# Kernel optimization log

Hardware: AMD Instinct MI355X
Metric: run time of the kernel (lower is better)

## Reference

```python
import jax, jax.numpy as jnp
import numpy as np

N, E, F, H, G, C = 50000, 600000, 128, 128, 500, 10
BN_EPS = 1e-5

def setup_inputs() -> dict:
    key = jax.random.key(0)
    ks = jax.random.split(key, 20)
    def lin(k, fan_in, shape):
        b = 1.0 / np.sqrt(fan_in)
        return jax.random.uniform(k, shape, jnp.float32, -b, b)
    inp = {
        'x': jax.random.normal(ks[0], (N, F), jnp.float32),
        'edge_index': jax.random.randint(ks[1], (2, E), 0, N, jnp.int64),
        'batch': jnp.sort(jax.random.randint(ks[2], (N,), 0, G, jnp.int64)),
        # conv1 MLP: Linear(F,H) -> BN(H) -> ReLU -> Dropout -> Linear(H,H) -> ReLU
        'W1a': lin(ks[3], F, (F, H)), 'b1a': lin(ks[4], F, (H,)),
        'g1': jnp.ones((H,), jnp.float32), 'be1': jnp.zeros((H,), jnp.float32),
        'm1': jnp.zeros((H,), jnp.float32), 'v1': jnp.ones((H,), jnp.float32),
        'W1b': lin(ks[5], H, (H, H)), 'b1b': lin(ks[6], H, (H,)),
        # conv2 MLP: Linear(H,H) -> ReLU -> BN(H) -> Dropout -> Linear(H,H) -> ReLU
        'W2a': lin(ks[7], H, (H, H)), 'b2a': lin(ks[8], H, (H,)),
        'g2': jnp.ones((H,), jnp.float32), 'be2': jnp.zeros((H,), jnp.float32),
        'm2': jnp.zeros((H,), jnp.float32), 'v2': jnp.ones((H,), jnp.float32),
        'W2b': lin(ks[9], H, (H, H)), 'b2b': lin(ks[10], H, (H,)),
        # heads
        'Wl1': lin(ks[11], 2 * H, (2 * H, H // 2)), 'bl1': lin(ks[12], 2 * H, (H // 2,)),
        'Wl2': lin(ks[13], H // 2, (H // 2, C)), 'bl2': lin(ks[14], H // 2, (C,)),
    }
    return inp

def _bn(h, g, b, m, v):
    return (h - m) * (g / jnp.sqrt(v + BN_EPS)) + b

def _gin_aggregate(x, src, dst):
    # out[i] = x[i] + sum_{j->i} x[j]  (GINConv with eps=0)
    return x + jax.ops.segment_sum(x[src], dst, num_segments=N)

def reference(x, edge_index, batch,
              W1a, b1a, g1, be1, m1, v1, W1b, b1b,
              W2a, b2a, g2, be2, m2, v2, W2b, b2b,
              Wl1, bl1, Wl2, bl2):
    src, dst = edge_index[0], edge_index[1]
    # conv1
    a1 = _gin_aggregate(x, src, dst)                       # [N, F]
    h1 = _bn(a1 @ W1a + b1a, g1, be1, m1, v1)
    h1 = jax.nn.relu(h1)                                   # dropout = identity (eval)
    h1 = jax.nn.relu(h1 @ W1b + b1b)                       # [N, H]
    # conv2
    a2 = _gin_aggregate(h1, src, dst)                      # [N, H]
    h2 = jax.nn.relu(a2 @ W2a + b2a)
    h2 = _bn(h2, g2, be2, m2, v2)
    h2 = jax.nn.relu(h2 @ W2b + b2b)                       # [N, H]
    # global add pool per graph
    p1 = jax.ops.segment_sum(h1, batch, num_segments=G)    # [G, H]
    p2 = jax.ops.segment_sum(h2, batch, num_segments=G)    # [G, H]
    z = jnp.concatenate((p1, p2), axis=1)                  # [G, 2H]
    z = jax.nn.relu(z @ Wl1 + bl1)
    return z @ Wl2 + bl2                                   # [G, C]
```

## Files before the change

kernel.cpp:

```cpp
#include <hip/hip_runtime.h>

#define N_NODES 50000
#define N_EDGES 600000
#define HDIM 128
#define NGRAPH 500
#define NCLASS 10
#define BN_EPS 1e-5f
#define KSLOT 64
#define KSTRIDE 72

typedef short short8 __attribute__((ext_vector_type(8)));
typedef unsigned short ushort8v __attribute__((ext_vector_type(8)));
typedef float floatx4 __attribute__((ext_vector_type(4)));

__device__ __forceinline__ float bf2f(unsigned short u) {
    unsigned int v = ((unsigned int)u) << 16;
    return __uint_as_float(v);
}
__device__ __forceinline__ unsigned short f2bf(float f) {
    unsigned int u = __float_as_uint(f);
    unsigned int r = (u + 0x7fffu + ((u >> 16) & 1u)) >> 16;
    return (unsigned short)r;
}

__global__ void k_zero(int* __restrict__ cnt) {
    int i = blockIdx.x * blockDim.x + threadIdx.x;
    if (i < N_NODES) cnt[i] = 0;
}

#define ILV 13
#define NB_SCAT 586
#define NB_CAST 6250
#define NB_PREPW 256
#define NB_POOLZ 500
#define NB_SETUP (NB_SCAT * ILV)

__global__ void k_setup(const float* __restrict__ x, unsigned short* __restrict__ xb,
                        const int* __restrict__ src, const int* __restrict__ dst,
                        int* __restrict__ cnt, unsigned short* __restrict__ adj,
                        float* __restrict__ pool,
                        const float* __restrict__ W1a, const float* __restrict__ W1b,
                        const float* __restrict__ W2a, const float* __restrict__ W2b,
                        unsigned short* __restrict__ wpack,
                        const float* __restrict__ b1a, const float* __restrict__ g1,
                        const float* __restrict__ be1, const float* __restrict__ m1,
                        const float* __restrict__ v1, const float* __restrict__ b1b,
                        const float* __restrict__ b2a, const float* __restrict__ g2,
                        const float* __restrict__ be2, const float* __restrict__ m2,
                        const float* __restrict__ v2, const float* __restrict__ b2b,
                        float* __restrict__ ep) {
    int b = blockIdx.x;
    int t = threadIdx.x;
    if (b % ILV == 0) {
        int i4 = (b / ILV) * 256 + t;
        if (i4 < N_EDGES / 4) {
            int4 s4 = ((const int4*)src)[i4];
            int4 d4 = ((const int4*)dst)[i4];
            int p;
            p = atomicAdd(&cnt[d4.x], 1); if (p < KSLOT) adj[d4.x * KSTRIDE + p] = (unsigned short)s4.x;
            p = atomicAdd(&cnt[d4.y], 1); if (p < KSLOT) adj[d4.y * KSTRIDE + p] = (unsigned short)s4.y;
            p = atomicAdd(&cnt[d4.z], 1); if (p < KSLOT) adj[d4.z * KSTRIDE + p] = (unsigned short)s4.z;
            p = atomicAdd(&cnt[d4.w], 1); if (p < KSLOT) adj[d4.w * KSTRIDE + p] = (unsigned short)s4.w;
        }
        return;
    }
    b = b - b / ILV - 1;
    if (b < NB_CAST) {
        int i = b * 256 + t;
        float4 v = ((const float4*)x)[i];
        ushort4 o;
        o.x = f2bf(v.x); o.y = f2bf(v.y); o.z = f2bf(v.z); o.w = f2bf(v.w);
        ((ushort4*)xb)[i] = o;
        return;
    }
    b -= NB_CAST;
    if (b < NB_PREPW) {
        int e = b * 256 + t;
        int w = e >> 14;
        int s_ = e & 16383;
        int j = s_ & 7;
        int m = (s_ >> 3) & 15;
        int q = (s_ >> 7) & 3;
        int ks = (s_ >> 9) & 3;
        int ct = (s_ >> 11) & 7;
        int n = ct * 16 + m;
        int k;
        float scale = 1.f;
        if (w == 0 || w == 2) {
            k = ks * 32 + q * 8 + j;
        } else {
            k = (ks * 2 + (j >> 2)) * 16 + q * 4 + (j & 3);
            if (w == 3) scale = g2[k] * rsqrtf(v2[k] + BN_EPS);
        }
        const float* W = (w == 0) ? W1a : (w == 1) ? W1b : (w == 2) ? W2a : W2b;
        wpack[e] = f2bf(W[k * 128 + n] * scale);
        return;
    }
    b -= NB_PREPW;
    if (b < NB_POOLZ) {
        int i = b * 256 + t;
        pool[i] = 0.f;
        return;
    }
    b -= NB_POOLZ;
    if (b != 0) return;
    if (t < 128) {
        int j = t;
        float s1 = g1[j] * rsqrtf(v1[j] + BN_EPS);
        ep[0 * 256 + 0 + j]   = s1;
        ep[0 * 256 + 128 + j] = (b1a[j] - m1[j]) * s1 + be1[j];
        ep[1 * 256 + 0 + j]   = 1.f;
        ep[1 * 256 + 128 + j] = b2a[j];
        ep[512 + j] = b1b[j];
        float acc = b2b[j];
        for (int k = 0; k < 128; k++) {
            float s2k = g2[k] * rsqrtf(v2[k] + BN_EPS);
            acc += (be2[k] - m2[k] * s2k) * W2b[k * 128 + j];
        }
        ep[512 + 128 + j] = acc;
    }
}

__global__ __launch_bounds__(256) void k_agg(const unsigned short* __restrict__ x,
                                             const int* __restrict__ cnt,
                                             const unsigned short* __restrict__ adj,
                                             unsigned short* __restrict__ out) {
    int g = blockIdx.x * 256 + threadIdx.x;
    int node = g >> 4;
    int m = g & 15;
    if (node >= N_NODES) return;

    int len = cnt[node];
    if (len > KSLOT) len = KSLOT;
    const unsigned short* ad = adj + node * KSTRIDE;

    ushort8v ra = *(const ushort8v*)(ad);

    float self[8];
    {
        short8 sv = *(const short8*)(x + (size_t)node * 128 + m * 8);
        #pragma unroll
        for (int j = 0; j < 8; j++) self[j] = bf2f((unsigned short)sv[j]);
    }
    float acc[8];
    #pragma unroll
    for (int j = 0; j < 8; j++) acc[j] = self[j];

    int nb = (len + 7) >> 3;
    for (int b = 0; b < nb; b++) {
        int i = b * 8;
        ushort8v na = *(const ushort8v*)(ad + i + 8);
        int u0 = (i + 0 < len) ? (int)ra[0] : node;
        int u1 = (i + 1 < len) ? (int)ra[1] : node;
        int u2 = (i + 2 < len) ? (int)ra[2] : node;
        int u3 = (i + 3 < len) ? (int)ra[3] : node;
        int u4 = (i + 4 < len) ? (int)ra[4] : node;
        int u5 = (i + 5 < len) ? (int)ra[5] : node;
        int u6 = (i + 6 < len) ? (int)ra[6] : node;
        int u7 = (i + 7 < len) ? (int)ra[7] : node;
        short8 f0 = *(const short8*)(x + (size_t)u0 * 128 + m * 8);
        short8 f1 = *(const short8*)(x + (size_t)u1 * 128 + m * 8);
        short8 f2 = *(const short8*)(x + (size_t)u2 * 128 + m * 8);
        short8 f3 = *(const short8*)(x + (size_t)u3 * 128 + m * 8);
        short8 f4 = *(const short8*)(x + (size_t)u4 * 128 + m * 8);
        short8 f5 = *(const short8*)(x + (size_t)u5 * 128 + m * 8);
        short8 f6 = *(const short8*)(x + (size_t)u6 * 128 + m * 8);
        short8 f7 = *(const short8*)(x + (size_t)u7 * 128 + m * 8);
        #pragma unroll
        for (int j = 0; j < 8; j++) {
            float a = bf2f((unsigned short)f0[j]) + bf2f((unsigned short)f1[j]) +
                      bf2f((unsigned short)f2[j]) + bf2f((unsigned short)f3[j]);
            float c = bf2f((unsigned short)f4[j]) + bf2f((unsigned short)f5[j]) +
                      bf2f((unsigned short)f6[j]) + bf2f((unsigned short)f7[j]);
            acc[j] += a + c;
        }
        ra = na;
    }
    float extra = (float)(nb * 8 - len);
    #pragma unroll
    for (int j = 0; j < 8; j++) acc[j] -= extra * self[j];

    short8 r;
    #pragma unroll
    for (int j = 0; j < 8; j++) r[j] = (short)f2bf(acc[j]);
    *(short8*)(out + (size_t)node * 128 + m * 8) = r;
}

__global__ __launch_bounds__(256, 2) void k_mlp(const unsigned short* __restrict__ A,
                                                const unsigned short* __restrict__ WaP,
                                                const unsigned short* __restrict__ WbP,
                                                const float* __restrict__ epi,
                                                const float* __restrict__ epf,
                                                const int* __restrict__ batch,
                                                float* __restrict__ poolc,
                                                unsigned short* __restrict__ Out, int n) {
    __shared__ unsigned short Wl[2][16384];
    __shared__ float ps[16][132];
    int t = threadIdx.x;
    int lane = t & 63;
    int w = t >> 6;
    int q = lane >> 4;
    int m = lane & 15;

    int rowbase0 = blockIdx.x * 64;
    int base = rowbase0 + w * 16;
    int node = base + m;
    if (node >= n) node = n - 1;

    short8 a1[4];
    #pragma unroll
    for (int s = 0; s < 4; s++)
        a1[s] = *(const short8*)(A + (size_t)node * 128 + s * 32 + q * 8);

    #pragma unroll
    for (int i = 0; i < 8; i++) {
        int c = t + 256 * i;
        *(short8*)(&Wl[0][c * 8]) = *(const short8*)(WaP + c * 8);
        *(short8*)(&Wl[1][c * 8]) = *(const short8*)(WbP + c * 8);
    }
    __syncthreads();

    int lbase = lane * 8;

    floatx4 acc1[8];
    #pragma unroll
    for (int c = 0; c < 8; c++) acc1[c] = (floatx4)0.f;
    #pragma unroll
    for (int s = 0; s < 4; s++) {
        #pragma unroll
        for (int ct = 0; ct < 8; ct++) {
            short8 wf = *(const short8*)(&Wl[0][(ct * 4 + s) * 512 + lbase]);
            acc1[ct] = __builtin_amdgcn_mfma_f32_16x16x32_bf16(wf, a1[s], acc1[ct], 0, 0, 0);
        }
    }

    short8 a2[4];
    #pragma unroll
    for (int s = 0; s < 4; s++) {
        #pragma unroll
        for (int j = 0; j < 8; j++) {
            int ct = s * 2 + (j >> 2);
            int r = j & 3;
            int col = ct * 16 + q * 4 + r;
            float P = epi[col], Q = epi[128 + col];
            float v = fmaxf(fmaf(acc1[ct][r], P, Q), 0.f);
            a2[s][j] = (short)f2bf(v);
        }
    }

    floatx4 acc2[8];
    #pragma unroll
    for (int c = 0; c < 8; c++) acc2[c] = (floatx4)0.f;
    #pragma unroll
    for (int s = 0; s < 4; s++) {
        #pragma unroll
        for (int ct = 0; ct < 8; ct++) {
            short8 wf = *(const short8*)(&Wl[1][(ct * 4 + s) * 512 + lbase]);
            acc2[ct] = __builtin_amdgcn_mfma_f32_16x16x32_bf16(a2[s], wf, acc2[ct], 0, 0, 0);
        }
    }

    #pragma unroll
    for (int ct = 0; ct < 8; ct++) {
        float Qf = epf[ct * 16 + m];
        #pragma unroll
        for (int r = 0; r < 4; r++) acc2[ct][r] = fmaxf(acc2[ct][r] + Qf, 0.f);
    }

    if (Out) {
        #pragma unroll
        for (int ct = 0; ct < 8; ct++) {
            int col = ct * 16 + m;
            #pragma unroll
            for (int r = 0; r < 4; r++) {
                int gr = base + q * 4 + r;
                if (gr < n)
                    Out[(size_t)gr * 128 + col] = f2bf(acc2[ct][r]);
            }
        }
    }

    int mygid[4];
    #pragma unroll
    for (int r = 0; r < 4; r++) {
        int gr = base + q * 4 + r;
        mygid[r] = (gr < n) ? batch[gr] : -1;
    }
    int lastrow = rowbase0 + 63;
    if (lastrow > n - 1) lastrow = n - 1;
    int g0 = batch[rowbase0];
    int g1 = batch[lastrow];
    for (int g = g0; g <= g1; g++) {
        float pv[8];
        #pragma unroll
        for (int ct = 0; ct < 8; ct++) pv[ct] = 0.f;
        #pragma unroll
        for (int r = 0; r < 4; r++) {
            if (mygid[r] == g) {
                #pragma unroll
                for (int ct = 0; ct < 8; ct++) pv[ct] += acc2[ct][r];
            }
        }
        #pragma unroll
        for (int ct = 0; ct < 8; ct++) ps[w * 4 + q][ct * 16 + m] = pv[ct];
        __syncthreads();
        if (t < 128) {
            float s = 0.f;
            #pragma unroll
            for (int k = 0; k < 16; k++) s += ps[k][t];
            atomicAdd(&poolc[g * 256 + t], s);
        }
        __syncthreads();
    }
}

__global__ void k_head(const float* __restrict__ pool, const float* __restrict__ Wl1,
                       const float* __restrict__ bl1, const float* __restrict__ Wl2,
                       const float* __restrict__ bl2, float* __restrict__ out) {
    int g = blockIdx.x;
    int t = threadIdx.x;
    __shared__ float zmid[64];
    const float* z = pool + g * 256;
    float acc = bl1[t];
    #pragma unroll 8
    for (int k = 0; k < 256; k++) acc = fmaf(z[k], Wl1[k * 64 + t], acc);
    zmid[t] = fmaxf(acc, 0.f);
    __syncthreads();
    if (t < NCLASS) {
        float a = bl2[t];
        #pragma unroll
        for (int j = 0; j < 64; j++) a = fmaf(zmid[j], Wl2[j * 10 + t], a);
        out[g * NCLASS + t] = a;
    }
}


extern "C" void kernel_launch(void* const* d_in, const int* in_sizes, int n_in,
                              void* d_out, int out_size, void* d_ws, size_t ws_size,
                              hipStream_t stream) {
    const float* x   = (const float*)d_in[0];
    const int* eidx  = (const int*)d_in[1];
    const int* batch = (const int*)d_in[2];
    const float* W1a = (const float*)d_in[3];
    const float* b1a = (const float*)d_in[4];
    const float* g1  = (const float*)d_in[5];
    const float* be1 = (const float*)d_in[6];
    const float* m1  = (const float*)d_in[7];
    const float* v1  = (const float*)d_in[8];
    const float* W1b = (const float*)d_in[9];
    const float* b1b = (const float*)d_in[10];
    const float* W2a = (const float*)d_in[11];
    const float* b2a = (const float*)d_in[12];
    const float* g2  = (const float*)d_in[13];
    const float* be2 = (const float*)d_in[14];
    const float* m2  = (const float*)d_in[15];
    const float* v2  = (const float*)d_in[16];
    const float* W2b = (const float*)d_in[17];
    const float* b2b = (const float*)d_in[18];
    const float* Wl1 = (const float*)d_in[19];
    const float* bl1 = (const float*)d_in[20];
    const float* Wl2 = (const float*)d_in[21];
    const float* bl2 = (const float*)d_in[22];
    const int* srcv = eidx;
    const int* dstv = eidx + N_EDGES;

    char* ws = (char*)d_ws;
    size_t off = 0;
    auto alloc = [&](size_t bytes) -> void* {
        void* p = ws + off;
        off = (off + bytes + 255) & ~(size_t)255;
        return p;
    };
    int* cnt      = (int*)alloc(sizeof(int) * N_NODES);
    unsigned short* adj = (unsigned short*)alloc(sizeof(unsigned short) * (size_t)N_NODES * KSTRIDE);
    float* ep     = (float*)alloc(sizeof(float) * 768);
    float* pool   = (float*)alloc(sizeof(float) * NGRAPH * 256);
    unsigned short* wpack = (unsigned short*)alloc(sizeof(unsigned short) * 4 * 16384);
    unsigned short* xb    = (unsigned short*)alloc(sizeof(unsigned short) * (size_t)N_NODES * HDIM);
    unsigned short* bufA  = (unsigned short*)alloc(sizeof(unsigned short) * (size_t)N_NODES * HDIM);
    unsigned short* bufC  = (unsigned short*)alloc(sizeof(unsigned short) * (size_t)N_NODES * HDIM);
    (void)ws_size; (void)in_sizes; (void)n_in; (void)out_size;

    float* outp = (float*)d_out;

    k_zero<<<dim3((N_NODES + 255) / 256), dim3(256), 0, stream>>>(cnt);
    k_setup<<<dim3(NB_SETUP), dim3(256), 0, stream>>>(
        x, xb, srcv, dstv, cnt, adj, pool, W1a, W1b, W2a, W2b, wpack,
        b1a, g1, be1, m1, v1, b1b, b2a, g2, be2, m2, v2, b2b, ep);

    dim3 agrid((N_NODES * 16 + 255) / 256), ablk(256);
    dim3 mgrid((N_NODES + 63) / 64), mblk(256);

    k_agg<<<agrid, ablk, 0, stream>>>(xb, cnt, adj, bufA);
    k_mlp<<<mgrid, mblk, 0, stream>>>(bufA, wpack + 0 * 16384, wpack + 1 * 16384,
                                      ep + 0, ep + 512, batch, pool + 0, bufC, N_NODES);
    k_agg<<<agrid, ablk, 0, stream>>>(bufC, cnt, adj, bufA);
    k_mlp<<<mgrid, mblk, 0, stream>>>(bufA, wpack + 2 * 16384, wpack + 3 * 16384,
                                      ep + 256, ep + 640, batch, pool + 128, nullptr, N_NODES);
    k_head<<<dim3(NGRAPH), dim3(64), 0, stream>>>(pool, Wl1, bl1, Wl2, bl2, outp);
}
```

Before: 229.2 us.

## Bucket adjacency lists by source range and batch four nodes per aggregation thread

Adjacency is now split into four buckets per destination, keyed on source node range, each holding at most 28 slots in a 128-entry row. The aggregation kernel runs a fixed grid of 1024 blocks, and each 16-lane group processes four destination nodes. It walks the buckets in order so that gathers across the wave hit similar source ranges, which is meant to improve cache locality and raise memory-level parallelism. The trade-offs are larger count and adjacency buffers, a per-bucket cap that can drop edges for skewed graphs, more registers per thread, and nontemporal output stores.

Measured after the change: 267.9 us. 1.17x slower.

```diff
diff --git a/kernel.cpp b/kernel.cpp
--- a/kernel.cpp
+++ b/kernel.cpp
@@ -6,8 +6,11 @@
 #define NGRAPH 500
 #define NCLASS 10
 #define BN_EPS 1e-5f
-#define KSLOT 64
-#define KSTRIDE 72
+
+#define NBUCK 4
+#define BSLOT 32
+#define BCAP 28
+#define AGG_BLOCKS 1024
 
 typedef short short8 __attribute__((ext_vector_type(8)));
 typedef unsigned short ushort8v __attribute__((ext_vector_type(8)));
@@ -25,7 +28,7 @@
 
 __global__ void k_zero(int* __restrict__ cnt) {
     int i = blockIdx.x * blockDim.x + threadIdx.x;
-    if (i < N_NODES) cnt[i] = 0;
+    if (i < N_NODES * NBUCK) cnt[i] = 0;
 }
 
 #define ILV 13
@@ -56,11 +59,19 @@
         if (i4 < N_EDGES / 4) {
             int4 s4 = ((const int4*)src)[i4];
             int4 d4 = ((const int4*)dst)[i4];
-            int p;
-            p = atomicAdd(&cnt[d4.x], 1); if (p < KSLOT) adj[d4.x * KSTRIDE + p] = (unsigned short)s4.x;
-            p = atomicAdd(&cnt[d4.y], 1); if (p < KSLOT) adj[d4.y * KSTRIDE + p] = (unsigned short)s4.y;
-            p = atomicAdd(&cnt[d4.z], 1); if (p < KSLOT) adj[d4.z * KSTRIDE + p] = (unsigned short)s4.z;
-            p = atomicAdd(&cnt[d4.w], 1); if (p < KSLOT) adj[d4.w * KSTRIDE + p] = (unsigned short)s4.w;
+            int p; unsigned bb;
+            bb = ((unsigned)s4.x * 5243u) >> 26;
+            p = atomicAdd(&cnt[d4.x * NBUCK + bb], 1);
+            if (p < BCAP) adj[(size_t)d4.x * 128 + bb * BSLOT + p] = (unsigned short)s4.x;
+            bb = ((unsigned)s4.y * 5243u) >> 26;
+            p = atomicAdd(&cnt[d4.y * NBUCK + bb], 1);
+            if (p < BCAP) adj[(size_t)d4.y * 128 + bb * BSLOT + p] = (unsigned short)s4.y;
+            bb = ((unsigned)s4.z * 5243u) >> 26;
+            p = atomicAdd(&cnt[d4.z * NBUCK + bb], 1);
+            if (p < BCAP) adj[(size_t)d4.z * 128 + bb * BSLOT + p] = (unsigned short)s4.z;
+            bb = ((unsigned)s4.w * 5243u) >> 26;
+            p = atomicAdd(&cnt[d4.w * NBUCK + bb], 1);
+            if (p < BCAP) adj[(size_t)d4.w * 128 + bb * BSLOT + p] = (unsigned short)s4.w;
         }
         return;
     }
@@ -121,69 +132,126 @@
     }
 }
 
-__global__ __launch_bounds__(256) void k_agg(const unsigned short* __restrict__ x,
-                                             const int* __restrict__ cnt,
-                                             const unsigned short* __restrict__ adj,
-                                             unsigned short* __restrict__ out) {
-    int g = blockIdx.x * 256 + threadIdx.x;
-    int node = g >> 4;
-    int m = g & 15;
-    if (node >= N_NODES) return;
-
-    int len = cnt[node];
-    if (len > KSLOT) len = KSLOT;
-    const unsigned short* ad = adj + node * KSTRIDE;
-
-    ushort8v ra = *(const ushort8v*)(ad);
-
-    float self[8];
-    {
-        short8 sv = *(const short8*)(x + (size_t)node * 128 + m * 8);
-        #pragma unroll
-        for (int j = 0; j < 8; j++) self[j] = bf2f((unsigned short)sv[j]);
-    }
-    float acc[8];
-    #pragma unroll
-    for (int j = 0; j < 8; j++) acc[j] = self[j];
-
-    int nb = (len + 7) >> 3;
-    for (int b = 0; b < nb; b++) {
-        int i = b * 8;
-        ushort8v na = *(const ushort8v*)(ad + i + 8);
-        int u0 = (i + 0 < len) ? (int)ra[0] : node;
-        int u1 = (i + 1 < len) ? (int)ra[1] : node;
-        int u2 = (i + 2 < len) ? (int)ra[2] : node;
-        int u3 = (i + 3 < len) ? (int)ra[3] : node;
-        int u4 = (i + 4 < len) ? (int)ra[4] : node;
-        int u5 = (i + 5 < len) ? (int)ra[5] : node;
-        int u6 = (i + 6 < len) ? (int)ra[6] : node;
-        int u7 = (i + 7 < len) ? (int)ra[7] : node;
-        short8 f0 = *(const short8*)(x + (size_t)u0 * 128 + m * 8);
-        short8 f1 = *(const short8*)(x + (size_t)u1 * 128 + m * 8);
-        short8 f2 = *(const short8*)(x + (size_t)u2 * 128 + m * 8);
-        short8 f3 = *(const short8*)(x + (size_t)u3 * 128 + m * 8);
-        short8 f4 = *(const short8*)(x + (size_t)u4 * 128 + m * 8);
-        short8 f5 = *(const short8*)(x + (size_t)u5 * 128 + m * 8);
-        short8 f6 = *(const short8*)(x + (size_t)u6 * 128 + m * 8);
-        short8 f7 = *(const short8*)(x + (size_t)u7 * 128 + m * 8);
+__global__ __launch_bounds__(256, 4) void k_agg(const unsigned short* __restrict__ x,
+                                                const int* __restrict__ cnt,
+                                                const unsigned short* __restrict__ adj,
+                                                unsigned short* __restrict__ out) {
+    int lg = threadIdx.x >> 4;
+    int m = threadIdx.x & 15;
+
+    int nd[4];
+    int lenk[4][4];
+    float acc[4][8];
+    int proc[4];
+
+    #pragma unroll
+    for (int k = 0; k < 4; k++) {
+        int n = (blockIdx.x + k * AGG_BLOCKS) * 16 + lg;
+        bool v = (n < N_NODES);
+        nd[k] = v ? n : 0;
+        int c0 = 0, c1 = 0, c2 = 0, c3 = 0;
+        if (v) {
+            int4 c = ((const int4*)cnt)[nd[k]];
+            c0 = min(c.x, BCAP); c1 = min(c.y, BCAP);
+            c2 = min(c.z, BCAP); c3 = min(c.w, BCAP);
+        }
+        lenk[k][0] = c0; lenk[k][1] = c1; lenk[k][2] = c2; lenk[k][3] = c3;
+        short8 sv = *(const short8*)(x + (size_t)nd[k] * 128 + m * 8);
+        #pragma unroll
+        for (int j = 0; j < 8; j++) acc[k][j] = bf2f((unsigned short)sv[j]);
+        proc[k] = 0;
+    }
+
+    #pragma unroll
+    for (int b = 0; b < 4; b++) {
+        #pragma unroll
+        for (int p2 = 0; p2 < 2; p2++) {
+            const int kA = 2 * p2, kB = 2 * p2 + 1;
+            int lA = lenk[kA][b], lB = lenk[kB][b];
+            if ((lA | lB) != 0) {
+                const unsigned short* aA = adj + (size_t)nd[kA] * 128 + b * BSLOT;
+                const unsigned short* aB = adj + (size_t)nd[kB] * 128 + b * BSLOT;
+                ushort4 rA = *(const ushort4*)aA;
+                ushort4 rB = *(const ushort4*)aB;
+                int u0 = (0 < lA) ? (int)rA.x : nd[kA];
+                int u1 = (1 < lA) ? (int)rA.y : nd[kA];
+                int u2 = (2 < lA) ? (int)rA.z : nd[kA];
+                int u3 = (3 < lA) ? (int)rA.w : nd[kA];
+                int u4 = (0 < lB) ? (int)rB.x : nd[kB];
+                int u5 = (1 < lB) ? (int)rB.y : nd[kB];
+                int u6 = (2 < lB) ? (int)rB.z : nd[kB];
+                int u7 = (3 < lB) ? (int)rB.w : nd[kB];
+                short8 f0 = *(const short8*)(x + (size_t)u0 * 128 + m * 8);
+                short8 f1 = *(const short8*)(x + (size_t)u1 * 128 + m * 8);
+                short8 f2 = *(const short8*)(x + (size_t)u2 * 128 + m * 8);
+                short8 f3 = *(const short8*)(x + (size_t)u3 * 128 + m * 8);
+                short8 f4 = *(const short8*)(x + (size_t)u4 * 128 + m * 8);
+                short8 f5 = *(const short8*)(x + (size_t)u5 * 128 + m * 8);
+                short8 f6 = *(const short8*)(x + (size_t)u6 * 128 + m * 8);
+                short8 f7 = *(const short8*)(x + (size_t)u7 * 128 + m * 8);
+                #pragma unroll
+                for (int j = 0; j < 8; j++) {
+                    float a = bf2f((unsigned short)f0[j]) + bf2f((unsigned short)f1[j]) +
+                              bf2f((unsigned short)f2[j]) + bf2f((unsigned short)f3[j]);
+                    float c = bf2f((unsigned short)f4[j]) + bf2f((unsigned short)f5[j]) +
+                              bf2f((unsigned short)f6[j]) + bf2f((unsigned short)f7[j]);
+                    acc[kA][j] += a;
+                    acc[kB][j] += c;
+                }
+                proc[kA] += 4;
+                proc[kB] += 4;
+                for (int i = 4; i < lA; i += 4) {
+                    ushort4 rn = *(const ushort4*)(aA + i);
+                    int w0 = (i + 0 < lA) ? (int)rn.x : nd[kA];
+                    int w1 = (i + 1 < lA) ? (int)rn.y : nd[kA];
+                    int w2 = (i + 2 < lA) ? (int)rn.z : nd[kA];
+                    int w3 = (i + 3 < lA) ? (int)rn.w : nd[kA];
+                    short8 t0 = *(const short8*)(x + (size_t)w0 * 128 + m * 8);
+                    short8 t1 = *(const short8*)(x + (size_t)w1 * 128 + m * 8);
+                    short8 t2 = *(const short8*)(x + (size_t)w2 * 128 + m * 8);
+                    short8 t3 = *(const short8*)(x + (size_t)w3 * 128 + m * 8);
+                    #pragma unroll
+                    for (int j = 0; j < 8; j++)
+                        acc[kA][j] += bf2f((unsigned short)t0[j]) + bf2f((unsigned short)t1[j]) +
+                                      bf2f((unsigned short)t2[j]) + bf2f((unsigned short)t3[j]);
+                    proc[kA] += 4;
+                }
+                for (int i = 4; i < lB; i += 4) {
+                    ushort4 rn = *(const ushort4*)(aB + i);
+                    int w0 = (i + 0 < lB) ? (int)rn.x : nd[kB];
+                    int w1 = (i + 1 < lB) ? (int)rn.y : nd[kB];
+                    int w2 = (i + 2 < lB) ? (int)rn.z : nd[kB];
+                    int w3 = (i + 3 < lB) ? (int)rn.w : nd[kB];
+                    short8 t0 = *(const short8*)(x + (size_t)w0 * 128 + m * 8);
+                    short8 t1 = *(const short8*)(x + (size_t)w1 * 128 + m * 8);
+                    short8 t2 = *(const short8*)(x + (size_t)w2 * 128 + m * 8);
+                    short8 t3 = *(const short8*)(x + (size_t)w3 * 128 + m * 8);
+                    #pragma unroll
+                    for (int j = 0; j < 8; j++)
+                        acc[kB][j] += bf2f((unsigned short)t0[j]) + bf2f((unsigned short)t1[j]) +
+                                      bf2f((unsigned short)t2[j]) + bf2f((unsigned short)t3[j]);
+                    proc[kB] += 4;
+                }
+            }
+        }
+        __builtin_amdgcn_sched_barrier(0);
+    }
+
+    #pragma unroll
+    for (int k = 0; k < 4; k++) {
+        int n = (blockIdx.x + k * AGG_BLOCKS) * 16 + lg;
+        if (n >= N_NODES) continue;
+        short8 sv = *(const short8*)(x + (size_t)n * 128 + m * 8);
+        int used = lenk[k][0] + lenk[k][1] + lenk[k][2] + lenk[k][3];
+        float extra = (float)(proc[k] - used);
+        short8 r;
         #pragma unroll
         for (int j = 0; j < 8; j++) {
-            float a = bf2f((unsigned short)f0[j]) + bf2f((unsigned short)f1[j]) +
-                      bf2f((unsigned short)f2[j]) + bf2f((unsigned short)f3[j]);
-            float c = bf2f((unsigned short)f4[j]) + bf2f((unsigned short)f5[j]) +
-                      bf2f((unsigned short)f6[j]) + bf2f((unsigned short)f7[j]);
-            acc[j] += a + c;
-        }
-        ra = na;
-    }
-    float extra = (float)(nb * 8 - len);
-    #pragma unroll
-    for (int j = 0; j < 8; j++) acc[j] -= extra * self[j];
-
-    short8 r;
-    #pragma unroll
-    for (int j = 0; j < 8; j++) r[j] = (short)f2bf(acc[j]);
-    *(short8*)(out + (size_t)node * 128 + m * 8) = r;
+            float s = bf2f((unsigned short)sv[j]);
+            r[j] = (short)f2bf(acc[k][j] - extra * s);
+        }
+        __builtin_nontemporal_store(r, (short8*)(out + (size_t)n * 128 + m * 8));
+    }
 }
 
 __global__ __launch_bounds__(256, 2) void k_mlp(const unsigned short* __restrict__ A,
@@ -371,8 +439,8 @@
         off = (off + bytes + 255) & ~(size_t)255;
         return p;
     };
-    int* cnt      = (int*)alloc(sizeof(int) * N_NODES);
-    unsigned short* adj = (unsigned short*)alloc(sizeof(unsigned short) * (size_t)N_NODES * KSTRIDE);
+    int* cnt      = (int*)alloc(sizeof(int) * N_NODES * NBUCK);
+    unsigned short* adj = (unsigned short*)alloc(sizeof(unsigned short) * (size_t)N_NODES * 128);
     float* ep     = (float*)alloc(sizeof(float) * 768);
     float* pool   = (float*)alloc(sizeof(float) * NGRAPH * 256);
     unsigned short* wpack = (unsigned short*)alloc(sizeof(unsigned short) * 4 * 16384);
@@ -383,12 +451,12 @@
 
     float* outp = (float*)d_out;
 
-    k_zero<<<dim3((N_NODES + 255) / 256), dim3(256), 0, stream>>>(cnt);
+    k_zero<<<dim3((N_NODES * NBUCK + 255) / 256), dim3(256), 0, stream>>>(cnt);
     k_setup<<<dim3(NB_SETUP), dim3(256), 0, stream>>>(
         x, xb, srcv, dstv, cnt, adj, pool, W1a, W1b, W2a, W2b, wpack,
         b1a, g1, be1, m1, v1, b1b, b2a, g2, be2, m2, v2, b2b, ep);
 
-    dim3 agrid((N_NODES * 16 + 255) / 256), ablk(256);
+    dim3 agrid(AGG_BLOCKS), ablk(256);
     dim3 mgrid((N_NODES + 63) / 64), mblk(256);
 
     k_agg<<<agrid, ablk, 0, stream>>>(xb, cnt, adj, bufA);
```
